# Kernel optimization log

Measured on AMD Instinct MI355X. Metric: run time of the kernel, lower is better.

Reference implementation:

```python
import jax, jax.numpy as jnp
import numpy as np

B, N, DIM = 8, 1024, 512
HEADS, DIM_HEAD = 8, 64
INNER = HEADS * DIM_HEAD  # 512


def setup_inputs() -> dict:
    key = jax.random.key(0)
    k1, k2, k3 = jax.random.split(key, 3)
    x = jax.random.normal(k1, (B, N, DIM), dtype=jnp.float32)
    # lecun-normal-ish scaling for dense weights
    w_qkv = jax.random.normal(k2, (DIM, INNER * 3), dtype=jnp.float32) / np.sqrt(DIM)
    w_out = jax.random.normal(k3, (INNER, DIM), dtype=jnp.float32) / np.sqrt(INNER)
    b_out = jnp.zeros((DIM,), dtype=jnp.float32)
    # learnable temperature initialized to log(dim_head ** -0.5)
    temperature = jnp.array(np.log(DIM_HEAD ** -0.5), dtype=jnp.float32)
    return {"x": x, "w_qkv": w_qkv, "temperature": temperature,
            "w_out": w_out, "b_out": b_out}


def reference(x, w_qkv, temperature, w_out, b_out):
    b, n, _ = x.shape
    scale = jnp.exp(temperature)
    qkv = x @ w_qkv  # (b, n, 3*inner)
    q, k, v = jnp.split(qkv, 3, axis=-1)
    # (b, n, h*d) -> (b, h, n, d)
    def split_heads(t):
        return t.reshape(b, n, HEADS, DIM_HEAD).transpose(0, 2, 1, 3)
    q, k, v = split_heads(q), split_heads(k), split_heads(v)
    dots = jnp.einsum('bhid,bhjd->bhij', q, k) * scale  # (b, h, n, n)
    mask = jnp.eye(n, dtype=bool)[None, None]
    dots = jnp.where(mask, jnp.finfo(dots.dtype).min, dots)
    attn = jax.nn.softmax(dots, axis=-1)
    out = jnp.einsum('bhij,bhjd->bhid', attn, v)  # (b, h, n, d)
    out = out.transpose(0, 2, 1, 3).reshape(b, n, INNER)
    return out @ w_out + b_out
```

## Files before the change

kernel.cpp:

```cpp
#include <hip/hip_runtime.h>


typedef __attribute__((ext_vector_type(8))) short    short8;
typedef __attribute__((ext_vector_type(8))) __bf16   bf16x8;
typedef __attribute__((ext_vector_type(4))) float    floatx4;
typedef __attribute__((ext_vector_type(4))) unsigned uint4v;
typedef __attribute__((ext_vector_type(2))) unsigned uint2v;

#define DEV static __device__ __forceinline__
#define AS1 __attribute__((address_space(1)))
#define AS3 __attribute__((address_space(3)))

DEV unsigned fbits(float f) { union { float f; unsigned u; } v; v.f = f; return v.u; }
DEV short f2bf_r(float f) {
    return (short)((fbits(f) + 0x8000u) >> 16);
}
DEV unsigned pack2r(float a, float b) {
    return __builtin_amdgcn_perm(fbits(b) + 0x8000u, fbits(a) + 0x8000u, 0x07060302u);
}
DEV floatx4 mfma16(short8 a, short8 b, floatx4 c) {
    return __builtin_amdgcn_mfma_f32_16x16x32_bf16(
        __builtin_bit_cast(bf16x8, a), __builtin_bit_cast(bf16x8, b), c, 0, 0, 0);
}
DEV void async16(const void* g, void* l) {
    __builtin_amdgcn_global_load_lds((AS1 void*)(unsigned long long)g,
                                     (AS3 void*)l, 16, 0, 0);
}

__global__ void prep(const float* __restrict__ x, const float* __restrict__ wqkv,
                     const float* __restrict__ wout, short* __restrict__ Xb,
                     short* __restrict__ wt1, short* __restrict__ wt2) {
    const int bid = blockIdx.x, tid = threadIdx.x;
    if (bid < 2048) {
        int base = bid * 2048 + tid * 8;
        float4 f0 = *(const float4*)&x[base];
        float4 f1 = *(const float4*)&x[base + 4];
        uint4v s = { pack2r(f0.x, f0.y), pack2r(f0.z, f0.w),
                     pack2r(f1.x, f1.y), pack2r(f1.z, f1.w) };
        *(uint4v*)&Xb[base] = s;
        return;
    }
    __shared__ short Ts[64][65];
    int t = bid - 2048;
    const float* src; short* dst; int srcld, n0, k0;
    if (t < 192) { int tn = t % 24, tk = t / 24; n0 = tn * 64; k0 = tk * 64;
                   src = wqkv; srcld = 1536; dst = wt1; }
    else { t -= 192; int tn = t & 7, tk = t >> 3; n0 = tn * 64; k0 = tk * 64;
           src = wout; srcld = 512; dst = wt2; }
#pragma unroll
    for (int it = 0; it < 16; it++) {
        int idx = it * 256 + tid, rk = idx >> 6, cn = idx & 63;
        Ts[cn][rk] = f2bf_r(src[(k0 + rk) * srcld + n0 + cn]);
    }
    __syncthreads();
#pragma unroll
    for (int it = 0; it < 16; it++) {
        int idx = it * 256 + tid, rn = idx >> 6, ck = idx & 63;
        dst[(n0 + rn) * 512 + k0 + ck] = Ts[rn][ck];
    }
}

template<int MODE>
__global__ __launch_bounds__(256, 2)
void gemm128(const short* __restrict__ A, const short* __restrict__ Bt,
             const float* __restrict__ temp,
             short* __restrict__ Qb, short* __restrict__ Kb, short* __restrict__ Vtb,
             float* __restrict__ Op, const float* __restrict__ bias) {
    union SMem {
        struct { short As[128 * 64]; short Bs[128 * 64]; } t;
        short Ts[128 * 130];
    };
    __shared__ __align__(16) SMem sm;

    const int tid  = threadIdx.x;
    const int lane = tid & 63, w = tid >> 6;
    const int wr = (w >> 1) * 64, wc = (w & 1) * 64;
    const int l15 = lane & 15, quad = lane >> 4;
    const int m0 = blockIdx.x * 128, n0 = blockIdx.y * 128;

    floatx4 acc[4][4];
#pragma unroll
    for (int i = 0; i < 4; i++)
#pragma unroll
        for (int j = 0; j < 4; j++) acc[i][j] = (floatx4)0.f;

    const int sr = (tid >> 3), scc = tid & 7;
    for (int kt = 0; kt < 512; kt += 64) {
#pragma unroll
        for (int it = 0; it < 4; it++) {
            int r = it * 32 + sr;
            int gcol = kt + ((scc ^ (r & 7)) * 8);
            async16(&A[(m0 + r) * 512 + gcol], sm.t.As + (it * 256 + w * 64) * 8);
            async16(&Bt[(n0 + r) * 512 + gcol], sm.t.Bs + (it * 256 + w * 64) * 8);
        }
        __syncthreads();
#pragma unroll
        for (int k2 = 0; k2 < 2; k2++) {
            const int cS = ((k2 * 4 + quad) ^ (l15 & 7)) * 8;
            short8 af[4], bf[4];
#pragma unroll
            for (int i = 0; i < 4; i++) {
                af[i] = *(const short8*)&sm.t.As[(wr + i * 16 + l15) * 64 + cS];
                bf[i] = *(const short8*)&sm.t.Bs[(wc + i * 16 + l15) * 64 + cS];
            }
#pragma unroll
            for (int i = 0; i < 4; i++)
#pragma unroll
                for (int j = 0; j < 4; j++)
                    acc[i][j] = mfma16(af[i], bf[j], acc[i][j]);
        }
        __syncthreads();
    }

    if (MODE == 1) {
#pragma unroll
        for (int i = 0; i < 4; i++) {
            int mrow = m0 + wr + i * 16 + quad * 4;
#pragma unroll
            for (int j = 0; j < 4; j++) {
                int col = n0 + wc + j * 16 + l15;
                float b = bias[col];
#pragma unroll
                for (int r = 0; r < 4; r++)
                    Op[(mrow + r) * 512 + col] = acc[i][j][r] + b;
            }
        }
        return;
    }

    const int which = n0 >> 9;
    const float qs = (which == 0) ? __expf(temp[0]) * 1.44269504089f : 1.f;
    const bool isV = (which == 2);
#pragma unroll
    for (int i = 0; i < 4; i++)
#pragma unroll
        for (int j = 0; j < 4; j++) {
            int c  = wc + j * 16 + l15;
            int tt = wr + i * 16 + quad * 4;
#pragma unroll
            for (int r = 0; r < 4; r++) {
                short v = f2bf_r(acc[i][j][r] * qs);
                if (isV) sm.Ts[c * 130 + tt + r] = v;
                else     sm.Ts[(tt + r) * 130 + c] = v;
            }
        }
    __syncthreads();
    const int bb = m0 >> 10, tloc = m0 & 1023;
#pragma unroll
    for (int it = 0; it < 8; it++) {
        int s = it * 256 + tid;
        int a = s >> 4, b8 = s & 15;
        short8 v = *(const short8*)&sm.Ts[a * 130 + b8 * 8];
        if (isV) {
            int vcol = n0 - 1024 + a;
            int bh = bb * 8 + (vcol >> 6), d = vcol & 63;
            *(short8*)&Vtb[(bh * 64 + d) * 1024 + tloc + b8 * 8] = v;
        } else {
            int col = n0 + b8 * 8;
            int bh = bb * 8 + ((col >> 6) & 7), d0 = col & 63;
            short* dst = (which == 0) ? Qb : Kb;
            *(short8*)&dst[(bh * 1024 + tloc + a) * 64 + d0] = v;
        }
    }
}

__global__ __launch_bounds__(512, 4)
void attn_kernel(const short* __restrict__ Q, const short* __restrict__ Kb,
                 const short* __restrict__ Vt, short* __restrict__ O) {
    __shared__ __align__(16) short Ks[128 * 64];
    __shared__ __align__(16) short Vs[64 * 128];

    const int tid  = threadIdx.x;
    const int lane = tid & 63, w = tid >> 6;
    const int l15 = lane & 15, quad = lane >> 4;
    const int qt = blockIdx.x & 7, bh = blockIdx.x >> 3;
    const int qrow = qt * 128 + w * 16 + l15;

    const short* Qp = Q + (bh * 1024 + qrow) * 64;
    short8 qf[2];
    qf[0] = *(const short8*)&Qp[quad * 8];
    qf[1] = *(const short8*)&Qp[32 + quad * 8];

    floatx4 accO[4];
#pragma unroll
    for (int di = 0; di < 4; di++) accO[di] = (floatx4)0.f;
    float lsum = 0.f;
    const int srcA = (quad & 1) * 32 + l15, srcB = srcA + 16;
    const bool hi = (quad & 2) != 0;
    const short* Kbase = Kb + bh * 1024 * 64;
    const short* Vbase = Vt + bh * 64 * 1024;

    for (int j = 0; j < 8; j++) {
        const int kv0 = j * 128;
#pragma unroll
        for (int it = 0; it < 2; it++) {
            int slot = it * 512 + tid;
            int rk = slot >> 3, ck = slot & 7;
            async16(&Kbase[(kv0 + rk) * 64 + ((ck ^ (rk & 7)) * 8)],
                    Ks + (it * 512 + w * 64) * 8);
            int rv = slot >> 4, cv = slot & 15;
            async16(&Vbase[rv * 1024 + kv0 + ((cv ^ (rv & 15)) * 8)],
                    Vs + (it * 512 + w * 64) * 8);
        }
        __syncthreads();

        floatx4 st[8];
#pragma unroll
        for (int ki = 0; ki < 8; ki++) st[ki] = (floatx4)0.f;
#pragma unroll
        for (int ki = 0; ki < 8; ki++) {
#pragma unroll
            for (int k2 = 0; k2 < 2; k2++) {
                const int cS = ((k2 * 4 + quad) ^ (l15 & 7)) * 8;
                short8 kf = *(const short8*)&Ks[(ki * 16 + l15) * 64 + cS];
                st[ki] = mfma16(kf, qf[k2], st[ki]);
            }
        }

        if (j == qt) {
#pragma unroll
            for (int ki = 0; ki < 8; ki++)
#pragma unroll
                for (int r = 0; r < 4; r++) {
                    int kv = kv0 + ki * 16 + quad * 4 + r;
                    if (kv == qrow) st[ki][r] = -3.0e38f;
                }
        }

#pragma unroll
        for (int ki = 0; ki < 8; ki++)
#pragma unroll
            for (int r = 0; r < 4; r++) {
                float p = exp2f(st[ki][r]);
                st[ki][r] = p;
                lsum += p;
            }

        unsigned u[8][2];
#pragma unroll
        for (int ki = 0; ki < 8; ki++) {
            u[ki][0] = pack2r(st[ki][0], st[ki][1]);
            u[ki][1] = pack2r(st[ki][2], st[ki][3]);
        }

#pragma unroll
        for (int k2 = 0; k2 < 4; k2++) {
            const int n0 = k2 * 2, n1 = n0 + 1;
            unsigned x0 = __shfl(u[n0][0], srcA), x1 = __shfl(u[n0][1], srcA);
            unsigned x2 = __shfl(u[n0][0], srcB), x3 = __shfl(u[n0][1], srcB);
            unsigned y0 = __shfl(u[n1][0], srcA), y1 = __shfl(u[n1][1], srcA);
            unsigned y2 = __shfl(u[n1][0], srcB), y3 = __shfl(u[n1][1], srcB);
            uint4v pu = { hi ? y0 : x0, hi ? y1 : x1, hi ? y2 : x2, hi ? y3 : x3 };
            short8 pa = __builtin_bit_cast(short8, pu);
#pragma unroll
            for (int di = 0; di < 4; di++) {
                const int cV = ((k2 * 4 + quad) ^ l15) * 8;
                short8 vf = *(const short8*)&Vs[(di * 16 + l15) * 128 + cV];
                accO[di] = mfma16(vf, pa, accO[di]);
            }
        }
        __syncthreads();
    }

    lsum += __shfl_xor(lsum, 16);
    lsum += __shfl_xor(lsum, 32);

    const int b = bh >> 3, h = bh & 7;
    const int token = b * 1024 + qrow;
    const float inv = 1.f / lsum;
#pragma unroll
    for (int di = 0; di < 4; di++) {
        uint2v s2 = { pack2r(accO[di][0] * inv, accO[di][1] * inv),
                      pack2r(accO[di][2] * inv, accO[di][3] * inv) };
        *(uint2v*)&O[token * 512 + h * 64 + di * 16 + quad * 4] = s2;
    }
}

extern "C" void kernel_launch(void* const* d_in, const int* in_sizes, int n_in,
                              void* d_out, int out_size, void* d_ws, size_t ws_size,
                              hipStream_t stream) {
    const float* x    = (const float*)d_in[0];
    const float* wqkv = (const float*)d_in[1];
    const float* temp = (const float*)d_in[2];
    const float* wout = (const float*)d_in[3];
    const float* bout = (const float*)d_in[4];
    float* out = (float*)d_out;

    short* ws  = (short*)d_ws;
    short* wt1 = ws;
    short* wt2 = wt1 + 786432;
    short* Qb  = wt2 + 262144;
    short* Kb  = Qb  + 4194304;
    short* Vtb = Kb  + 4194304;
    short* Xb  = Vtb + 4194304;
    short* Ob  = Xb;

    prep<<<2304, 256, 0, stream>>>(x, wqkv, wout, Xb, wt1, wt2);

    dim3 g1(64, 12);
    gemm128<0><<<g1, 256, 0, stream>>>(Xb, wt1, temp, Qb, Kb, Vtb, nullptr, nullptr);

    attn_kernel<<<512, 512, 0, stream>>>(Qb, Kb, Vtb, Ob);

    dim3 g2(64, 4);
    gemm128<1><<<g2, 256, 0, stream>>>(Ob, wt2, nullptr, nullptr, nullptr, nullptr, out, bout);
}
```

Before: 149.7 us.

## Switch attention kernel to 32x32x16 MFMA with 4 waves per block

Rewrites the attention kernel to use 32x32x16 bf16 MFMA instead of 16x16x32. Each wave now owns 32 query rows, so a block needs only 256 threads. The P-to-operand transpose shrinks to one xor-32 shuffle per pair, and K/V are staged in padded 528-element LDS groups with XOR swizzles. The goal is fewer LDS reads and shuffles per FLOP, and better MFMA throughput from the larger tile. The cost is more accumulator registers per wave and half as many waves per block, which can lower occupancy and latency hiding.

New measurement: 142.3 us. 1.05x faster.

```diff
diff --git a/kernel.cpp b/kernel.cpp
--- a/kernel.cpp
+++ b/kernel.cpp
@@ -1,11 +1,12 @@
 #include <hip/hip_runtime.h>
 
 
-typedef __attribute__((ext_vector_type(8))) short    short8;
-typedef __attribute__((ext_vector_type(8))) __bf16   bf16x8;
-typedef __attribute__((ext_vector_type(4))) float    floatx4;
-typedef __attribute__((ext_vector_type(4))) unsigned uint4v;
-typedef __attribute__((ext_vector_type(2))) unsigned uint2v;
+typedef __attribute__((ext_vector_type(8)))  short    short8;
+typedef __attribute__((ext_vector_type(8)))  __bf16   bf16x8;
+typedef __attribute__((ext_vector_type(4)))  float    floatx4;
+typedef __attribute__((ext_vector_type(16))) float    floatx16;
+typedef __attribute__((ext_vector_type(4)))  unsigned uint4v;
+typedef __attribute__((ext_vector_type(2)))  unsigned uint2v;
 
 #define DEV static __device__ __forceinline__
 #define AS1 __attribute__((address_space(1)))
@@ -20,6 +21,10 @@
 }
 DEV floatx4 mfma16(short8 a, short8 b, floatx4 c) {
     return __builtin_amdgcn_mfma_f32_16x16x32_bf16(
+        __builtin_bit_cast(bf16x8, a), __builtin_bit_cast(bf16x8, b), c, 0, 0, 0);
+}
+DEV floatx16 mfma32(short8 a, short8 b, floatx16 c) {
+    return __builtin_amdgcn_mfma_f32_32x32x16_bf16(
         __builtin_bit_cast(bf16x8, a), __builtin_bit_cast(bf16x8, b), c, 0, 0, 0);
 }
 DEV void async16(const void* g, void* l) {
@@ -164,116 +169,103 @@
     }
 }
 
-__global__ __launch_bounds__(512, 4)
+__global__ __launch_bounds__(256, 3)
 void attn_kernel(const short* __restrict__ Q, const short* __restrict__ Kb,
                  const short* __restrict__ Vt, short* __restrict__ O) {
-    __shared__ __align__(16) short Ks[128 * 64];
-    __shared__ __align__(16) short Vs[64 * 128];
+    __shared__ __align__(16) short Ks[16 * 528];
+    __shared__ __align__(16) short Vs[16 * 528];
 
     const int tid  = threadIdx.x;
     const int lane = tid & 63, w = tid >> 6;
-    const int l15 = lane & 15, quad = lane >> 4;
+    const int l31 = lane & 31, h = lane >> 5;
     const int qt = blockIdx.x & 7, bh = blockIdx.x >> 3;
-    const int qrow = qt * 128 + w * 16 + l15;
+    const int qrow = qt * 128 + w * 32 + l31;
 
     const short* Qp = Q + (bh * 1024 + qrow) * 64;
-    short8 qf[2];
-    qf[0] = *(const short8*)&Qp[quad * 8];
-    qf[1] = *(const short8*)&Qp[32 + quad * 8];
-
-    floatx4 accO[4];
-#pragma unroll
-    for (int di = 0; di < 4; di++) accO[di] = (floatx4)0.f;
+    short8 qf[4];
+#pragma unroll
+    for (int ks = 0; ks < 4; ks++)
+        qf[ks] = *(const short8*)&Qp[ks * 16 + h * 8];
+
+    floatx16 accO[2];
+    accO[0] = (floatx16)0.f; accO[1] = (floatx16)0.f;
     float lsum = 0.f;
-    const int srcA = (quad & 1) * 32 + l15, srcB = srcA + 16;
-    const bool hi = (quad & 2) != 0;
-    const short* Kbase = Kb + bh * 1024 * 64;
-    const short* Vbase = Vt + bh * 64 * 1024;
+
+    const unsigned lanemask =
+        (h == ((l31 >> 2) & 1)) ? (1u << ((l31 & 3) | (((l31 >> 3) & 3) << 2))) : 0u;
+
+    const int krow_off = lane >> 3, kchunk = ((lane & 7) ^ (lane >> 3)) * 8;
+    const int vrow_off = lane >> 4, vcs = lane & 15;
+    const short* Kbase = Kb + bh * 65536;
+    const short* Vbase = Vt + bh * 65536;
 
     for (int j = 0; j < 8; j++) {
         const int kv0 = j * 128;
 #pragma unroll
-        for (int it = 0; it < 2; it++) {
-            int slot = it * 512 + tid;
-            int rk = slot >> 3, ck = slot & 7;
-            async16(&Kbase[(kv0 + rk) * 64 + ((ck ^ (rk & 7)) * 8)],
-                    Ks + (it * 512 + w * 64) * 8);
-            int rv = slot >> 4, cv = slot & 15;
-            async16(&Vbase[rv * 1024 + kv0 + ((cv ^ (rv & 15)) * 8)],
-                    Vs + (it * 512 + w * 64) * 8);
-        }
-        __syncthreads();
-
-        floatx4 st[8];
-#pragma unroll
-        for (int ki = 0; ki < 8; ki++) st[ki] = (floatx4)0.f;
-#pragma unroll
-        for (int ki = 0; ki < 8; ki++) {
-#pragma unroll
-            for (int k2 = 0; k2 < 2; k2++) {
-                const int cS = ((k2 * 4 + quad) ^ (l15 & 7)) * 8;
-                short8 kf = *(const short8*)&Ks[(ki * 16 + l15) * 64 + cS];
-                st[ki] = mfma16(kf, qf[k2], st[ki]);
-            }
-        }
-
-        if (j == qt) {
-#pragma unroll
-            for (int ki = 0; ki < 8; ki++)
-#pragma unroll
-                for (int r = 0; r < 4; r++) {
-                    int kv = kv0 + ki * 16 + quad * 4 + r;
-                    if (kv == qrow) st[ki][r] = -3.0e38f;
-                }
-        }
-
-#pragma unroll
-        for (int ki = 0; ki < 8; ki++)
-#pragma unroll
-            for (int r = 0; r < 4; r++) {
-                float p = exp2f(st[ki][r]);
-                st[ki][r] = p;
-                lsum += p;
-            }
-
-        unsigned u[8][2];
-#pragma unroll
-        for (int ki = 0; ki < 8; ki++) {
-            u[ki][0] = pack2r(st[ki][0], st[ki][1]);
-            u[ki][1] = pack2r(st[ki][2], st[ki][3]);
-        }
-
-#pragma unroll
-        for (int k2 = 0; k2 < 4; k2++) {
-            const int n0 = k2 * 2, n1 = n0 + 1;
-            unsigned x0 = __shfl(u[n0][0], srcA), x1 = __shfl(u[n0][1], srcA);
-            unsigned x2 = __shfl(u[n0][0], srcB), x3 = __shfl(u[n0][1], srcB);
-            unsigned y0 = __shfl(u[n1][0], srcA), y1 = __shfl(u[n1][1], srcA);
-            unsigned y2 = __shfl(u[n1][0], srcB), y3 = __shfl(u[n1][1], srcB);
-            uint4v pu = { hi ? y0 : x0, hi ? y1 : x1, hi ? y2 : x2, hi ? y3 : x3 };
-            short8 pa = __builtin_bit_cast(short8, pu);
-#pragma unroll
-            for (int di = 0; di < 4; di++) {
-                const int cV = ((k2 * 4 + quad) ^ l15) * 8;
-                short8 vf = *(const short8*)&Vs[(di * 16 + l15) * 128 + cV];
-                accO[di] = mfma16(vf, pa, accO[di]);
-            }
-        }
-        __syncthreads();
-    }
-
-    lsum += __shfl_xor(lsum, 16);
+        for (int it = 0; it < 4; it++) {
+            int g = it * 4 + w;
+            async16(&Kbase[(kv0 + g * 8 + krow_off) * 64 + kchunk], Ks + g * 528);
+            int vr = g * 4 + vrow_off;
+            async16(&Vbase[vr * 1024 + kv0 + ((vcs ^ (vr & 15)) * 8)], Vs + g * 528);
+        }
+        __syncthreads();
+
+        unsigned u[32];
+#pragma unroll
+        for (int sub = 0; sub < 4; sub++) {
+            floatx16 sacc = (floatx16)0.f;
+#pragma unroll
+            for (int ks = 0; ks < 4; ks++) {
+                const int grp = sub * 4 + (l31 >> 3);
+                const int ck = ((2 * ks + h) ^ (l31 & 7)) * 8;
+                short8 kf = *(const short8*)&Ks[grp * 528 + (l31 & 7) * 64 + ck];
+                sacc = mfma32(kf, qf[ks], sacc);
+            }
+            if (j == qt && sub == w) {
+#pragma unroll
+                for (int r = 0; r < 16; r++)
+                    if ((lanemask >> r) & 1) sacc[r] = -3.0e38f;
+            }
+#pragma unroll
+            for (int r2 = 0; r2 < 8; r2++) {
+                float p0 = exp2f(sacc[2 * r2]), p1 = exp2f(sacc[2 * r2 + 1]);
+                lsum += p0 + p1;
+                u[sub * 8 + r2] = pack2r(p0, p1);
+            }
+        }
+
+#pragma unroll
+        for (int s = 0; s < 8; s++) {
+            const int i0 = 8 * (s >> 1) + 4 * (s & 1);
+            unsigned sA = h ? u[i0] : u[i0 + 2], sB = h ? u[i0 + 1] : u[i0 + 3];
+            unsigned rA = __shfl_xor(sA, 32), rB = __shfl_xor(sB, 32);
+            uint4v pu = { h ? rA : u[i0],     h ? rB : u[i0 + 1],
+                          h ? u[i0 + 2] : rA, h ? u[i0 + 3] : rB };
+            short8 pf = __builtin_bit_cast(short8, pu);
+#pragma unroll
+            for (int dt = 0; dt < 2; dt++) {
+                const int gv = dt * 8 + (l31 >> 2);
+                const int cv = ((2 * s + h) ^ (l31 & 15)) * 8;
+                short8 vf = *(const short8*)&Vs[gv * 528 + (l31 & 3) * 128 + cv];
+                accO[dt] = mfma32(vf, pf, accO[dt]);
+            }
+        }
+        __syncthreads();
+    }
+
     lsum += __shfl_xor(lsum, 32);
-
-    const int b = bh >> 3, h = bh & 7;
+    const float inv = 1.f / lsum;
+
+    const int b = bh >> 3, head = bh & 7;
     const int token = b * 1024 + qrow;
-    const float inv = 1.f / lsum;
-#pragma unroll
-    for (int di = 0; di < 4; di++) {
-        uint2v s2 = { pack2r(accO[di][0] * inv, accO[di][1] * inv),
-                      pack2r(accO[di][2] * inv, accO[di][3] * inv) };
-        *(uint2v*)&O[token * 512 + h * 64 + di * 16 + quad * 4] = s2;
-    }
+#pragma unroll
+    for (int dt = 0; dt < 2; dt++)
+#pragma unroll
+        for (int g = 0; g < 4; g++) {
+            uint2v s2 = { pack2r(accO[dt][4 * g] * inv, accO[dt][4 * g + 1] * inv),
+                          pack2r(accO[dt][4 * g + 2] * inv, accO[dt][4 * g + 3] * inv) };
+            *(uint2v*)&O[token * 512 + head * 64 + dt * 32 + 8 * g + 4 * h] = s2;
+        }
 }
 
 extern "C" void kernel_launch(void* const* d_in, const int* in_sizes, int n_in,
@@ -300,7 +292,7 @@
     dim3 g1(64, 12);
     gemm128<0><<<g1, 256, 0, stream>>>(Xb, wt1, temp, Qb, Kb, Vtb, nullptr, nullptr);
 
-    attn_kernel<<<512, 512, 0, stream>>>(Qb, Kb, Vtb, Ob);
+    attn_kernel<<<512, 256, 0, stream>>>(Qb, Kb, Vtb, Ob);
 
     dim3 g2(64, 4);
     gemm128<1><<<g2, 256, 0, stream>>>(Ob, wt2, nullptr, nullptr, nullptr, nullptr, out, bout);
```
